# Kernel optimization log

Measured on AMD Instinct MI355X. Metric: run time of the kernel, lower is better.

Reference implementation:

```python
import jax, jax.numpy as jnp
import numpy as np

D_MODEL = 1024
NUM_HEADS = 16
D_K = D_MODEL // NUM_HEADS


def setup_inputs() -> dict:
    key = jax.random.key(0)
    ks = jax.random.split(key, 13)
    B, S = 2, 2048
    s = 1.0 / np.sqrt(D_MODEL)
    inp = {
        'q': jax.random.normal(ks[0], (B, S, D_MODEL), jnp.float32),
        'k': jax.random.normal(ks[1], (B, S, D_MODEL), jnp.float32),
        'v': jax.random.normal(ks[2], (B, S, D_MODEL), jnp.float32),
        'mask': jax.random.randint(ks[3], (B, S), 0, 2, jnp.int32),
        'Wq': jax.random.normal(ks[4], (D_MODEL, D_MODEL), jnp.float32) * s,
        'bq': jax.random.normal(ks[5], (D_MODEL,), jnp.float32) * s,
        'Wk': jax.random.normal(ks[6], (D_MODEL, D_MODEL), jnp.float32) * s,
        'bk': jax.random.normal(ks[7], (D_MODEL,), jnp.float32) * s,
        'Wv': jax.random.normal(ks[8], (D_MODEL, D_MODEL), jnp.float32) * s,
        'bv': jax.random.normal(ks[9], (D_MODEL,), jnp.float32) * s,
        'Wo': jax.random.normal(ks[10], (D_MODEL, D_MODEL), jnp.float32) * s,
        'bo': jax.random.normal(ks[11], (D_MODEL,), jnp.float32) * s,
    }
    return inp


def reference(q, k, v, mask, Wq, bq, Wk, bk, Wv, bv, Wo, bo):
    B, S, _ = q.shape

    def split(x):  # [B,S,D] -> [B,H,S,d_k]
        return x.reshape(B, -1, NUM_HEADS, D_K).transpose(0, 2, 1, 3)

    qh = split(q @ Wq.T + bq)
    kh = split(k @ Wk.T + bk)
    vh = split(v @ Wv.T + bv)

    scores = jnp.einsum('bhqd,bhkd->bhqk', qh, kh) / jnp.sqrt(jnp.float32(D_K))
    scores = jnp.where(mask[:, None, None, :] == 0, jnp.float32(-1e9), scores)
    attn = jax.nn.softmax(scores, axis=-1)
    out = jnp.einsum('bhqk,bhkd->bhqd', attn, vh)  # [B,H,S,d_k]
    out = out.transpose(0, 2, 1, 3).reshape(B, S, NUM_HEADS * D_K)
    return out @ Wo.T + bo
```

## Files before the change

### kernel.cpp

```cpp
#include <hip/hip_runtime.h>
#include <cstdint>
#include <cstddef>


using bf16   = __bf16;
using bf16x4 = __attribute__((ext_vector_type(4))) __bf16;
using bf16x8 = __attribute__((ext_vector_type(8))) __bf16;
using f32x4  = __attribute__((ext_vector_type(4))) float;

#define MFMA_BF16(a, b, c) __builtin_amdgcn_mfma_f32_16x16x32_bf16((a), (b), (c), 0, 0, 0)

__device__ __forceinline__ void gload_lds16(const void* g, void* l) {
  __builtin_amdgcn_global_load_lds((__attribute__((address_space(1))) void*)g,
                                   (__attribute__((address_space(3))) void*)l,
                                   16, 0, 0);
}

#define LOG2E 1.4426950408889634f

__global__ __launch_bounds__(256) void prep_kernel(
    const float* __restrict__ q, const float* __restrict__ k, const float* __restrict__ v,
    const int* __restrict__ mask,
    const float* __restrict__ Wq, const float* __restrict__ Wk,
    const float* __restrict__ Wv, const float* __restrict__ Wo,
    bf16* __restrict__ qb, bf16* __restrict__ kb, bf16* __restrict__ vb,
    bf16* __restrict__ Wqb, bf16* __restrict__ Wkb, bf16* __restrict__ Wvb,
    bf16* __restrict__ Wob, float* __restrict__ maskf)
{
  const int NQ = 1048576;
  const int NW = 262144;
  int i = blockIdx.x * 256 + threadIdx.x;
  if (i < 3 * NQ) {
    const float* src; bf16* dst; int j;
    if (i < NQ)        { src = q; dst = qb; j = i; }
    else if (i < 2*NQ) { src = k; dst = kb; j = i - NQ; }
    else               { src = v; dst = vb; j = i - 2*NQ; }
    float4 f = ((const float4*)src)[j];
    ((bf16x4*)dst)[j] = bf16x4{(bf16)f.x, (bf16)f.y, (bf16)f.z, (bf16)f.w};
  } else if (i < 3*NQ + 4*NW) {
    int j = i - 3*NQ;
    const float* src; bf16* dst;
    if (j < NW)        { src = Wq; dst = Wqb; }
    else if (j < 2*NW) { src = Wk; dst = Wkb; j -= NW; }
    else if (j < 3*NW) { src = Wv; dst = Wvb; j -= 2*NW; }
    else               { src = Wo; dst = Wob; j -= 3*NW; }
    float4 f = ((const float4*)src)[j];
    ((bf16x4*)dst)[j] = bf16x4{(bf16)f.x, (bf16)f.y, (bf16)f.z, (bf16)f.w};
  } else if (i < 3*NQ + 4*NW + 1024) {
    int j = i - 3*NQ - 4*NW;
    int4 mi = ((const int4*)mask)[j];
    float4 o;
    o.x = (mi.x == 0) ? -1e9f * LOG2E : 0.0f;
    o.y = (mi.y == 0) ? -1e9f * LOG2E : 0.0f;
    o.z = (mi.z == 0) ? -1e9f * LOG2E : 0.0f;
    o.w = (mi.w == 0) ? -1e9f * LOG2E : 0.0f;
    ((float4*)maskf)[j] = o;
  }
}

__device__ __forceinline__ void gemm128_core(const bf16* __restrict__ A,
                                             const bf16* __restrict__ Bw,
                                             int K, int m0, int n0,
                                             bf16* As, bf16* Bs, f32x4 acc[4][4])
{
  const int tid  = threadIdx.x;
  const int w    = tid >> 6;
  const int lane = tid & 63;
  const int wr = w >> 1, wc = w & 1;
  const int quad = lane >> 4, l16 = lane & 15;
  const int srow = lane >> 3;
  const int scol = (lane & 7) * 8;

#pragma unroll
  for (int mt = 0; mt < 4; ++mt)
#pragma unroll
    for (int nt = 0; nt < 4; ++nt)
      acc[mt][nt] = f32x4{0.f, 0.f, 0.f, 0.f};

  for (int k0 = 0; k0 < K; k0 += 64) {
#pragma unroll
    for (int c4 = 0; c4 < 4; ++c4) {
      const int c   = w * 4 + c4;
      const int row = c * 8 + srow;
      gload_lds16(A  + (size_t)(m0 + row) * K + k0 + scol, As + c * 512);
      gload_lds16(Bw + (size_t)(n0 + row) * K + k0 + scol, Bs + c * 512);
    }
    __syncthreads();
#pragma unroll
    for (int kk = 0; kk < 2; ++kk) {
      bf16x8 af[4], bfr[4];
#pragma unroll
      for (int mt = 0; mt < 4; ++mt)
        af[mt] = *(const bf16x8*)(As + (wr*64 + mt*16 + l16) * 64 + kk*32 + quad*8);
#pragma unroll
      for (int nt = 0; nt < 4; ++nt)
        bfr[nt] = *(const bf16x8*)(Bs + (wc*64 + nt*16 + l16) * 64 + kk*32 + quad*8);
#pragma unroll
      for (int mt = 0; mt < 4; ++mt)
#pragma unroll
        for (int nt = 0; nt < 4; ++nt)
          acc[mt][nt] = MFMA_BF16(af[mt], bfr[nt], acc[mt][nt]);
    }
    __syncthreads();
  }
}

__global__ __launch_bounds__(256) void proj3_kernel(
    const bf16* __restrict__ Xq, const bf16* __restrict__ Xk, const bf16* __restrict__ Xv,
    const bf16* __restrict__ Wqb, const bf16* __restrict__ Wkb, const bf16* __restrict__ Wvb,
    const float* __restrict__ bq, const float* __restrict__ bk, const float* __restrict__ bv,
    bf16* __restrict__ qh, bf16* __restrict__ kh, bf16* __restrict__ vhT)
{
  __shared__ bf16 As[128 * 64];
  __shared__ bf16 Bs[128 * 64];
  const int z = blockIdx.z;
  const bf16*  X    = (z == 0) ? Xq  : (z == 1) ? Xk  : Xv;
  const bf16*  Wb   = (z == 0) ? Wqb : (z == 1) ? Wkb : Wvb;
  const float* bias = (z == 0) ? bq  : (z == 1) ? bk  : bv;
  const int m0 = blockIdx.x * 128, n0 = blockIdx.y * 128;

  f32x4 acc[4][4];
  gemm128_core(X, Wb, 1024, m0, n0, As, Bs, acc);

  const int tid = threadIdx.x, w = tid >> 6, lane = tid & 63;
  const int wr = w >> 1, wc = w & 1, quad = lane >> 4, l16 = lane & 15;
#pragma unroll
  for (int mt = 0; mt < 4; ++mt) {
#pragma unroll
    for (int nt = 0; nt < 4; ++nt) {
      const int n = n0 + wc*64 + nt*16 + l16;
      const int h = n >> 6, d = n & 63;
      const float bn = bias[n];
#pragma unroll
      for (int r = 0; r < 4; ++r) {
        const int m  = m0 + wr*64 + mt*16 + quad*4 + r;
        const int bb = m >> 11, s = m & 2047;
        const float val = acc[mt][nt][r] + bn;
        if (z == 0)
          qh[(((size_t)bb*16 + h)*2048 + s)*64 + d] = (bf16)(val * (0.125f * LOG2E));
        else if (z == 1)
          kh[(((size_t)bb*16 + h)*2048 + s)*64 + d] = (bf16)val;
        else
          vhT[(((size_t)bb*16 + h)*64 + d)*2048 + s] = (bf16)val;
      }
    }
  }
}

#define PSTRIDE 72

__global__ __launch_bounds__(256, 2) void attn_kernel(
    const bf16* __restrict__ qh, const bf16* __restrict__ kh,
    const bf16* __restrict__ vhT, const float* __restrict__ maskf,
    bf16* __restrict__ out)
{
  __shared__ bf16 Ks[2][64 * 64];
  __shared__ bf16 Vs[2][64 * 64];
  __shared__ bf16 Ps[4][16 * PSTRIDE];

  const int tid = threadIdx.x, w = tid >> 6, lane = tid & 63;
  const int quad = lane >> 4, l16 = lane & 15;
  const int sw = l16 & 7;
  const int srow8  = lane >> 3;
  const int scol   = ((lane & 7) ^ srow8) * 8;

  const int L  = blockIdx.x;
  const int bh = (L & 7) + ((L >> 7) << 3);
  const int qt = (L >> 3) & 15;
  const int b  = bh >> 4, h = bh & 15;
  const int q0 = qt * 128 + w * 32;

  const bf16* kbase = kh  + (size_t)bh * 2048 * 64;
  const bf16* vbase = vhT + (size_t)bh * 64 * 2048;
  const bf16* qbase = qh  + ((size_t)bh * 2048 + q0) * 64;
  const float* mbase = maskf + (size_t)b * 2048;
  bf16* Pw = Ps[w];

  bf16x8 aQ[2][2];
#pragma unroll
  for (int rb = 0; rb < 2; ++rb)
#pragma unroll
    for (int kk = 0; kk < 2; ++kk)
      aQ[rb][kk] = *(const bf16x8*)(qbase + (size_t)(rb*16 + l16)*64 + kk*32 + quad*8);

  f32x4 Oacc[2][4];
  float lsum[2] = {0.f, 0.f};
#pragma unroll
  for (int rb = 0; rb < 2; ++rb)
#pragma unroll
    for (int mb = 0; mb < 4; ++mb) Oacc[rb][mb] = f32x4{0.f,0.f,0.f,0.f};

  auto stage = [&](int t, int buf) {
    const int kt0 = t * 64;
#pragma unroll
    for (int c2 = 0; c2 < 2; ++c2) {
      const int c   = w * 2 + c2;
      const int row = c * 8 + srow8;
      gload_lds16(kbase + (size_t)(kt0 + row) * 64 + scol, &Ks[buf][c * 512]);
      gload_lds16(vbase + (size_t)row * 2048 + kt0 + scol, &Vs[buf][c * 512]);
    }
  };

  stage(0, 0);
  float4 mk[4], mkn[4];
#pragma unroll
  for (int mb = 0; mb < 4; ++mb)
    mk[mb] = *(const float4*)(mbase + mb*16 + quad*4);

  for (int t = 0; t < 32; ++t) {
    const int cur = t & 1;
    __syncthreads();

    if (t < 31) {
      stage(t + 1, cur ^ 1);
      const int kt0n = (t + 1) * 64;
#pragma unroll
      for (int mb = 0; mb < 4; ++mb)
        mkn[mb] = *(const float4*)(mbase + kt0n + mb*16 + quad*4);
    }

    bf16x8 fK[8], fV[8];
#pragma unroll
    for (int mb = 0; mb < 4; ++mb)
#pragma unroll
      for (int kk = 0; kk < 2; ++kk) {
        const int off = (mb*16 + l16)*64 + ((kk*4 + quad) ^ sw)*8;
        fK[mb*2+kk] = *(const bf16x8*)(&Ks[cur][off]);
        fV[mb*2+kk] = *(const bf16x8*)(&Vs[cur][off]);
      }

#pragma unroll
    for (int rb = 0; rb < 2; ++rb) {
      f32x4 sac[4];
#pragma unroll
      for (int mb = 0; mb < 4; ++mb)
        sac[mb] = f32x4{mk[mb].x, mk[mb].y, mk[mb].z, mk[mb].w};
#pragma unroll
      for (int kk = 0; kk < 2; ++kk)
#pragma unroll
        for (int mb = 0; mb < 4; ++mb)
          sac[mb] = MFMA_BF16(fK[mb*2+kk], aQ[rb][kk], sac[mb]);

      float p[4][4];
#pragma unroll
      for (int mb = 0; mb < 4; ++mb)
#pragma unroll
        for (int r = 0; r < 4; ++r) {
          p[mb][r] = exp2f(sac[mb][r]);
          lsum[rb] += p[mb][r];
        }

#pragma unroll
      for (int mb = 0; mb < 4; ++mb) {
        bf16x4 pk = bf16x4{(bf16)p[mb][0], (bf16)p[mb][1], (bf16)p[mb][2], (bf16)p[mb][3]};
        *(bf16x4*)(Pw + l16*PSTRIDE + mb*16 + quad*4) = pk;
      }
#pragma unroll
      for (int kk = 0; kk < 2; ++kk) {
        bf16x8 aP = *(const bf16x8*)(Pw + l16*PSTRIDE + kk*32 + quad*8);
#pragma unroll
        for (int mb = 0; mb < 4; ++mb)
          Oacc[rb][mb] = MFMA_BF16(fV[mb*2+kk], aP, Oacc[rb][mb]);
      }
    }

#pragma unroll
    for (int mb = 0; mb < 4; ++mb) mk[mb] = mkn[mb];
  }

#pragma unroll
  for (int rb = 0; rb < 2; ++rb) {
    float l_ = lsum[rb];
    l_ += __shfl_xor(l_, 16);
    l_ += __shfl_xor(l_, 32);
    const float inv = 1.0f / l_;
#pragma unroll
    for (int mb = 0; mb < 4; ++mb) {
      bf16x4 o = bf16x4{(bf16)(Oacc[rb][mb][0]*inv), (bf16)(Oacc[rb][mb][1]*inv),
                        (bf16)(Oacc[rb][mb][2]*inv), (bf16)(Oacc[rb][mb][3]*inv)};
      *(bf16x4*)(out + ((size_t)b*2048 + q0 + rb*16 + l16)*1024 + h*64 + mb*16 + quad*4) = o;
    }
  }
}

__global__ __launch_bounds__(256) void oproj_kernel(
    const bf16* __restrict__ Ain, const bf16* __restrict__ Wob,
    const float* __restrict__ bo, float* __restrict__ out)
{
  __shared__ bf16 As[128 * 64];
  __shared__ bf16 Bs[128 * 64];
  const int m0 = blockIdx.x * 128, n0 = blockIdx.y * 128;
  f32x4 acc[4][4];
  gemm128_core(Ain, Wob, 1024, m0, n0, As, Bs, acc);

  const int tid = threadIdx.x, w = tid >> 6, lane = tid & 63;
  const int wr = w >> 1, wc = w & 1, quad = lane >> 4, l16 = lane & 15;
#pragma unroll
  for (int mt = 0; mt < 4; ++mt) {
#pragma unroll
    for (int nt = 0; nt < 4; ++nt) {
      const int n = n0 + wc*64 + nt*16 + l16;
      const float bn = bo[n];
#pragma unroll
      for (int r = 0; r < 4; ++r) {
        const int m = m0 + wr*64 + mt*16 + quad*4 + r;
        out[(size_t)m * 1024 + n] = acc[mt][nt][r] + bn;
      }
    }
  }
}

extern "C" void kernel_launch(void* const* d_in, const int* in_sizes, int n_in,
                              void* d_out, int out_size, void* d_ws, size_t ws_size,
                              hipStream_t stream)
{
  const float* q    = (const float*)d_in[0];
  const float* k    = (const float*)d_in[1];
  const float* v    = (const float*)d_in[2];
  const int*   mask = (const int*)d_in[3];
  const float* Wq   = (const float*)d_in[4];
  const float* bq   = (const float*)d_in[5];
  const float* Wk   = (const float*)d_in[6];
  const float* bk   = (const float*)d_in[7];
  const float* Wv   = (const float*)d_in[8];
  const float* bv   = (const float*)d_in[9];
  const float* Wo   = (const float*)d_in[10];
  const float* bo   = (const float*)d_in[11];

  char* ws = (char*)d_ws;
  bf16*  qb    = (bf16*)(ws);
  bf16*  kb    = (bf16*)(ws + (8ull  << 20));
  bf16*  vb    = (bf16*)(ws + (16ull << 20));
  bf16*  Wqb   = (bf16*)(ws + (24ull << 20));
  bf16*  Wkb   = (bf16*)(ws + (26ull << 20));
  bf16*  Wvb   = (bf16*)(ws + (28ull << 20));
  bf16*  Wob   = (bf16*)(ws + (30ull << 20));
  float* maskf = (float*)(ws + (32ull << 20));
  bf16*  qh    = (bf16*)(ws + (33ull << 20));
  bf16*  kh    = (bf16*)(ws + (41ull << 20));
  bf16*  vhT   = (bf16*)(ws + (49ull << 20));
  bf16*  ao    = (bf16*)(ws);
  float* out   = (float*)d_out;

  prep_kernel<<<16388, 256, 0, stream>>>(q, k, v, mask, Wq, Wk, Wv, Wo,
                                         qb, kb, vb, Wqb, Wkb, Wvb, Wob, maskf);
  proj3_kernel<<<dim3(32, 8, 3), 256, 0, stream>>>(qb, kb, vb, Wqb, Wkb, Wvb,
                                                   bq, bk, bv, qh, kh, vhT);
  attn_kernel<<<512, 256, 0, stream>>>(qh, kh, vhT, maskf, ao);
  oproj_kernel<<<dim3(32, 8), 256, 0, stream>>>(ao, Wob, bo, out);
}
```

Measured before the change: 263.5 us.

## Swizzle GEMM LDS, transpose V projection, shrink attention and out-proj tiles

Applies an XOR swizzle to the LDS staging in the shared GEMM core to avoid bank conflicts. The V projection is computed transposed so the vhT stores become contiguous along the sequence. Attention blocks are halved to 128 threads (64 queries) to double the grid size, and the row-sum is now computed with an MFMA against a ones vector instead of per-lane adds plus shuffles. The output projection uses 64x128 tiles to double its block count. The result is several unrelated tuning changes bundled together, and each may shift occupancy or load balance.

```diff
diff --git a/kernel.cpp b/kernel.cpp
--- a/kernel.cpp
+++ b/kernel.cpp
@@ -68,8 +68,9 @@
   const int lane = tid & 63;
   const int wr = w >> 1, wc = w & 1;
   const int quad = lane >> 4, l16 = lane & 15;
-  const int srow = lane >> 3;
-  const int scol = (lane & 7) * 8;
+  const int sw = l16 & 7;
+  const int srow8 = lane >> 3;
+  const int scol  = ((lane & 7) ^ srow8) * 8;
 
 #pragma unroll
   for (int mt = 0; mt < 4; ++mt)
@@ -81,7 +82,7 @@
 #pragma unroll
     for (int c4 = 0; c4 < 4; ++c4) {
       const int c   = w * 4 + c4;
-      const int row = c * 8 + srow;
+      const int row = c * 8 + srow8;
       gload_lds16(A  + (size_t)(m0 + row) * K + k0 + scol, As + c * 512);
       gload_lds16(Bw + (size_t)(n0 + row) * K + k0 + scol, Bs + c * 512);
     }
@@ -91,10 +92,10 @@
       bf16x8 af[4], bfr[4];
 #pragma unroll
       for (int mt = 0; mt < 4; ++mt)
-        af[mt] = *(const bf16x8*)(As + (wr*64 + mt*16 + l16) * 64 + kk*32 + quad*8);
+        af[mt] = *(const bf16x8*)(As + (wr*64 + mt*16 + l16) * 64 + ((kk*4 + quad) ^ sw) * 8);
 #pragma unroll
       for (int nt = 0; nt < 4; ++nt)
-        bfr[nt] = *(const bf16x8*)(Bs + (wc*64 + nt*16 + l16) * 64 + kk*32 + quad*8);
+        bfr[nt] = *(const bf16x8*)(Bs + (wc*64 + nt*16 + l16) * 64 + ((kk*4 + quad) ^ sw) * 8);
 #pragma unroll
       for (int mt = 0; mt < 4; ++mt)
 #pragma unroll
@@ -114,16 +115,37 @@
   __shared__ bf16 As[128 * 64];
   __shared__ bf16 Bs[128 * 64];
   const int z = blockIdx.z;
-  const bf16*  X    = (z == 0) ? Xq  : (z == 1) ? Xk  : Xv;
-  const bf16*  Wb   = (z == 0) ? Wqb : (z == 1) ? Wkb : Wvb;
-  const float* bias = (z == 0) ? bq  : (z == 1) ? bk  : bv;
   const int m0 = blockIdx.x * 128, n0 = blockIdx.y * 128;
-
-  f32x4 acc[4][4];
-  gemm128_core(X, Wb, 1024, m0, n0, As, Bs, acc);
 
   const int tid = threadIdx.x, w = tid >> 6, lane = tid & 63;
   const int wr = w >> 1, wc = w & 1, quad = lane >> 4, l16 = lane & 15;
+
+  f32x4 acc[4][4];
+
+  if (z == 2) {
+    gemm128_core(Wvb, Xv, 1024, n0, m0, As, Bs, acc);
+#pragma unroll
+    for (int mt = 0; mt < 4; ++mt) {
+#pragma unroll
+      for (int nt = 0; nt < 4; ++nt) {
+        const int tok = m0 + wc*64 + nt*16 + l16;
+        const int bb = tok >> 11, s = tok & 2047;
+#pragma unroll
+        for (int r = 0; r < 4; ++r) {
+          const int dv = n0 + wr*64 + mt*16 + quad*4 + r;
+          const int h = dv >> 6, d = dv & 63;
+          vhT[(((size_t)bb*16 + h)*64 + d)*2048 + s] = (bf16)(acc[mt][nt][r] + bv[dv]);
+        }
+      }
+    }
+    return;
+  }
+
+  const bf16*  X    = (z == 0) ? Xq  : Xk;
+  const bf16*  Wb   = (z == 0) ? Wqb : Wkb;
+  const float* bias = (z == 0) ? bq  : bk;
+  gemm128_core(X, Wb, 1024, m0, n0, As, Bs, acc);
+
 #pragma unroll
   for (int mt = 0; mt < 4; ++mt) {
 #pragma unroll
@@ -138,10 +160,8 @@
         const float val = acc[mt][nt][r] + bn;
         if (z == 0)
           qh[(((size_t)bb*16 + h)*2048 + s)*64 + d] = (bf16)(val * (0.125f * LOG2E));
-        else if (z == 1)
+        else
           kh[(((size_t)bb*16 + h)*2048 + s)*64 + d] = (bf16)val;
-        else
-          vhT[(((size_t)bb*16 + h)*64 + d)*2048 + s] = (bf16)val;
       }
     }
   }
@@ -149,26 +169,26 @@
 
 #define PSTRIDE 72
 
-__global__ __launch_bounds__(256, 2) void attn_kernel(
+__global__ __launch_bounds__(128) void attn_kernel(
     const bf16* __restrict__ qh, const bf16* __restrict__ kh,
     const bf16* __restrict__ vhT, const float* __restrict__ maskf,
     bf16* __restrict__ out)
 {
   __shared__ bf16 Ks[2][64 * 64];
   __shared__ bf16 Vs[2][64 * 64];
-  __shared__ bf16 Ps[4][16 * PSTRIDE];
+  __shared__ bf16 Ps[2][16 * PSTRIDE];
 
   const int tid = threadIdx.x, w = tid >> 6, lane = tid & 63;
   const int quad = lane >> 4, l16 = lane & 15;
   const int sw = l16 & 7;
-  const int srow8  = lane >> 3;
-  const int scol   = ((lane & 7) ^ srow8) * 8;
+  const int srow8 = lane >> 3;
+  const int scol  = ((lane & 7) ^ srow8) * 8;
 
   const int L  = blockIdx.x;
-  const int bh = (L & 7) + ((L >> 7) << 3);
-  const int qt = (L >> 3) & 15;
+  const int bh = (L & 7) + ((L >> 8) << 3);
+  const int qt = (L >> 3) & 31;
   const int b  = bh >> 4, h = bh & 15;
-  const int q0 = qt * 128 + w * 32;
+  const int q0 = qt * 64 + w * 32;
 
   const bf16* kbase = kh  + (size_t)bh * 2048 * 64;
   const bf16* vbase = vhT + (size_t)bh * 64 * 2048;
@@ -183,18 +203,23 @@
     for (int kk = 0; kk < 2; ++kk)
       aQ[rb][kk] = *(const bf16x8*)(qbase + (size_t)(rb*16 + l16)*64 + kk*32 + quad*8);
 
+  const bf16 one = (bf16)1.0f;
+  const bf16x8 aOnes = bf16x8{one, one, one, one, one, one, one, one};
+
   f32x4 Oacc[2][4];
-  float lsum[2] = {0.f, 0.f};
-#pragma unroll
-  for (int rb = 0; rb < 2; ++rb)
+  f32x4 lacc[2];
+#pragma unroll
+  for (int rb = 0; rb < 2; ++rb) {
+    lacc[rb] = f32x4{0.f,0.f,0.f,0.f};
 #pragma unroll
     for (int mb = 0; mb < 4; ++mb) Oacc[rb][mb] = f32x4{0.f,0.f,0.f,0.f};
+  }
 
   auto stage = [&](int t, int buf) {
     const int kt0 = t * 64;
 #pragma unroll
-    for (int c2 = 0; c2 < 2; ++c2) {
-      const int c   = w * 2 + c2;
+    for (int c4 = 0; c4 < 4; ++c4) {
+      const int c   = w * 4 + c4;
       const int row = c * 8 + srow8;
       gload_lds16(kbase + (size_t)(kt0 + row) * 64 + scol, &Ks[buf][c * 512]);
       gload_lds16(vbase + (size_t)row * 2048 + kt0 + scol, &Vs[buf][c * 512]);
@@ -245,10 +270,8 @@
 #pragma unroll
       for (int mb = 0; mb < 4; ++mb)
 #pragma unroll
-        for (int r = 0; r < 4; ++r) {
+        for (int r = 0; r < 4; ++r)
           p[mb][r] = exp2f(sac[mb][r]);
-          lsum[rb] += p[mb][r];
-        }
 
 #pragma unroll
       for (int mb = 0; mb < 4; ++mb) {
@@ -261,6 +284,7 @@
 #pragma unroll
         for (int mb = 0; mb < 4; ++mb)
           Oacc[rb][mb] = MFMA_BF16(fV[mb*2+kk], aP, Oacc[rb][mb]);
+        lacc[rb] = MFMA_BF16(aOnes, aP, lacc[rb]);
       }
     }
 
@@ -270,10 +294,7 @@
 
 #pragma unroll
   for (int rb = 0; rb < 2; ++rb) {
-    float l_ = lsum[rb];
-    l_ += __shfl_xor(l_, 16);
-    l_ += __shfl_xor(l_, 32);
-    const float inv = 1.0f / l_;
+    const float inv = 1.0f / lacc[rb][0];
 #pragma unroll
     for (int mb = 0; mb < 4; ++mb) {
       bf16x4 o = bf16x4{(bf16)(Oacc[rb][mb][0]*inv), (bf16)(Oacc[rb][mb][1]*inv),
@@ -287,23 +308,64 @@
     const bf16* __restrict__ Ain, const bf16* __restrict__ Wob,
     const float* __restrict__ bo, float* __restrict__ out)
 {
-  __shared__ bf16 As[128 * 64];
+  __shared__ bf16 As[64 * 64];
   __shared__ bf16 Bs[128 * 64];
-  const int m0 = blockIdx.x * 128, n0 = blockIdx.y * 128;
-  f32x4 acc[4][4];
-  gemm128_core(Ain, Wob, 1024, m0, n0, As, Bs, acc);
+  const int m0 = blockIdx.x * 64, n0 = blockIdx.y * 128;
 
   const int tid = threadIdx.x, w = tid >> 6, lane = tid & 63;
-  const int wr = w >> 1, wc = w & 1, quad = lane >> 4, l16 = lane & 15;
+  const int quad = lane >> 4, l16 = lane & 15;
+  const int sw = l16 & 7;
+  const int srow8 = lane >> 3;
+  const int scol  = ((lane & 7) ^ srow8) * 8;
+
+  f32x4 acc[4][2];
+#pragma unroll
+  for (int mt = 0; mt < 4; ++mt)
+#pragma unroll
+    for (int nt = 0; nt < 2; ++nt)
+      acc[mt][nt] = f32x4{0.f, 0.f, 0.f, 0.f};
+
+  for (int k0 = 0; k0 < 1024; k0 += 64) {
+#pragma unroll
+    for (int c4 = 0; c4 < 6; ++c4) {
+      const int c = w * 6 + c4;
+      if (c < 8) {
+        const int row = c * 8 + srow8;
+        gload_lds16(Ain + (size_t)(m0 + row) * 1024 + k0 + scol, As + c * 512);
+      } else {
+        const int cB = c - 8;
+        const int row = cB * 8 + srow8;
+        gload_lds16(Wob + (size_t)(n0 + row) * 1024 + k0 + scol, Bs + cB * 512);
+      }
+    }
+    __syncthreads();
+#pragma unroll
+    for (int kk = 0; kk < 2; ++kk) {
+      bf16x8 af[4], bfr[2];
+#pragma unroll
+      for (int mt = 0; mt < 4; ++mt)
+        af[mt] = *(const bf16x8*)(As + (mt*16 + l16) * 64 + ((kk*4 + quad) ^ sw) * 8);
+#pragma unroll
+      for (int nt = 0; nt < 2; ++nt)
+        bfr[nt] = *(const bf16x8*)(Bs + (w*32 + nt*16 + l16) * 64 + ((kk*4 + quad) ^ sw) * 8);
+#pragma unroll
+      for (int mt = 0; mt < 4; ++mt)
+#pragma unroll
+        for (int nt = 0; nt < 2; ++nt)
+          acc[mt][nt] = MFMA_BF16(af[mt], bfr[nt], acc[mt][nt]);
+    }
+    __syncthreads();
+  }
+
 #pragma unroll
   for (int mt = 0; mt < 4; ++mt) {
 #pragma unroll
-    for (int nt = 0; nt < 4; ++nt) {
-      const int n = n0 + wc*64 + nt*16 + l16;
+    for (int nt = 0; nt < 2; ++nt) {
+      const int n = n0 + w*32 + nt*16 + l16;
       const float bn = bo[n];
 #pragma unroll
       for (int r = 0; r < 4; ++r) {
-        const int m = m0 + wr*64 + mt*16 + quad*4 + r;
+        const int m = m0 + mt*16 + quad*4 + r;
         out[(size_t)m * 1024 + n] = acc[mt][nt][r] + bn;
       }
     }
@@ -346,6 +408,6 @@
                                          qb, kb, vb, Wqb, Wkb, Wvb, Wob, maskf);
   proj3_kernel<<<dim3(32, 8, 3), 256, 0, stream>>>(qb, kb, vb, Wqb, Wkb, Wvb,
                                                    bq, bk, bv, qh, kh, vhT);
-  attn_kernel<<<512, 256, 0, stream>>>(qh, kh, vhT, maskf, ao);
-  oproj_kernel<<<dim3(32, 8), 256, 0, stream>>>(ao, Wob, bo, out);
-}
+  attn_kernel<<<1024, 128, 0, stream>>>(qh, kh, vhT, maskf, ao);
+  oproj_kernel<<<dim3(64, 8), 256, 0, stream>>>(ao, Wob, bo, out);
+}
```

After: 258.1 us. -2.1%, faster.
